# Optimization experiments

Measured on AMD Instinct MI355X. Metric: run time of the kernel, lower is better.

## Reference

```python
import jax, jax.numpy as jnp
import numpy as np
import math

B, L, D, P = 2, 2048, 256, 32

def _lin_init(key, fan_in, shape):
    return jax.random.normal(key, shape, dtype=jnp.float32) / np.float32(math.sqrt(fan_in))

def setup_inputs() -> dict:
    key = jax.random.key(0)
    ks = jax.random.split(key, 16)
    return {
        "x": jax.random.normal(ks[0], (B, L, D), dtype=jnp.float32),
        "pos_phases": jax.random.normal(ks[1], (L, P), dtype=jnp.float32) * np.float32(math.pi),
        "w_pos_value": _lin_init(ks[2], D, (D, D)), "b_pos_value": jnp.zeros((D,), jnp.float32),
        "w_key": _lin_init(ks[3], D, (D, P)), "b_key": jnp.zeros((P,), jnp.float32),
        "w_kv": _lin_init(ks[4], D, (D, D)), "b_kv": jnp.zeros((D,), jnp.float32),
        "w_vg1": _lin_init(ks[5], 2 * D, (2 * D, D)), "b_vg1": jnp.zeros((D,), jnp.float32),
        "w_vg2": _lin_init(ks[6], D, (D, 1)), "b_vg2": jnp.zeros((1,), jnp.float32),
        "w_bg1": _lin_init(ks[7], D, (D, D // 2)), "b_bg1": jnp.zeros((D // 2,), jnp.float32),
        "w_bg2": _lin_init(ks[8], D // 2, (D // 2, 2)), "b_bg2": jnp.zeros((2,), jnp.float32),
        "ln_r_g": jnp.ones((D,), jnp.float32), "ln_r_b": jnp.zeros((D,), jnp.float32),
        "w_r1": _lin_init(ks[9], D, (D, 2 * D)), "b_r1": jnp.zeros((2 * D,), jnp.float32),
        "w_r2": _lin_init(ks[10], 2 * D, (2 * D, D)), "b_r2": jnp.zeros((D,), jnp.float32),
        "ln_o_g": jnp.ones((D,), jnp.float32), "ln_o_b": jnp.zeros((D,), jnp.float32),
        "w_out": _lin_init(ks[11], D, (D, D)), "b_out": jnp.zeros((D,), jnp.float32),
    }

def _ln(z, g, b, eps=1e-5):
    mu = z.mean(-1, keepdims=True)
    var = ((z - mu) ** 2).mean(-1, keepdims=True)
    return (z - mu) * jax.lax.rsqrt(var + eps) * g + b

def _shift1(z):
    # torch.roll(shifts=1, dims=1) then zero first position == shift right with zero pad
    return jnp.concatenate([jnp.zeros_like(z[:, :1]), z[:, :-1]], axis=1)

def reference(x, pos_phases, w_pos_value, b_pos_value, w_key, b_key, w_kv, b_kv,
              w_vg1, b_vg1, w_vg2, b_vg2, w_bg1, b_bg1, w_bg2, b_bg2,
              ln_r_g, ln_r_b, w_r1, b_r1, w_r2, b_r2, ln_o_g, ln_o_b, w_out, b_out):
    Bv, Lv, Dv = x.shape
    Pv = pos_phases.shape[1]
    inv_sqrt_p = np.float32(1.0 / math.sqrt(Pv))

    # --- positional memory ---
    pos_phasors = jnp.exp(1j * pos_phases)                      # (L,P) complex64
    pos_values = (x @ w_pos_value + b_pos_value).astype(jnp.complex64)  # (B,L,D)
    pos_bound = pos_phasors[None, :, :, None] * pos_values[:, :, None, :]  # (B,L,P,D)
    pos_memory = jnp.cumsum(pos_bound, axis=1)
    pos_query = jnp.exp(-1j * pos_phases)                       # (L,P)
    pos_retrieved = (pos_memory * pos_query[None, :, :, None]).sum(axis=2).real * inv_sqrt_p

    # --- content-based KV memory ---
    key_phases = jnp.tanh(x @ w_key + b_key) * np.float32(math.pi)  # (B,L,P)
    key_phasors = jnp.exp(1j * key_phases)
    kv_values = (x @ w_kv + b_kv).astype(jnp.complex64)         # (B,L,D)

    x_shifted = _shift1(x)
    gate_input = jnp.concatenate([x, x_shifted], axis=-1)       # (B,L,2D)
    h = jax.nn.gelu(gate_input @ w_vg1 + b_vg1, approximate=False)
    value_gates = jax.nn.sigmoid(h @ w_vg2 + b_vg2)             # (B,L,1)

    key_phasors_shifted = _shift1(key_phasors)                  # (B,L,P)
    kv_bound = (key_phasors_shifted[..., None] * kv_values[:, :, None, :]) \
               * value_gates[:, :, :, None].astype(jnp.complex64)  # (B,L,P,D)
    kv_memory = jnp.cumsum(kv_bound, axis=1)
    gate_cumsum = jnp.maximum(jnp.cumsum(value_gates, axis=1), 1.0)  # (B,L,1)
    kv_query = jnp.exp(-1j * key_phases)                        # (B,L,P)
    kv_retrieved = (kv_memory * kv_query[..., None]).sum(axis=2).real
    kv_retrieved = kv_retrieved / (jnp.sqrt(gate_cumsum) * np.float32(math.sqrt(Pv)))

    # --- blend, refine, output ---
    bg_h = jax.nn.gelu(x @ w_bg1 + b_bg1, approximate=False)
    blend = jax.nn.softmax(bg_h @ w_bg2 + b_bg2, axis=-1)       # (B,L,2)
    blended = blend[..., 0:1] * pos_retrieved + blend[..., 1:2] * kv_retrieved

    refined = jax.nn.gelu(_ln(blended, ln_r_g, ln_r_b) @ w_r1 + b_r1, approximate=False) @ w_r2 + b_r2
    return x + (_ln(refined, ln_o_g, ln_o_b) @ w_out + b_out)
```

## Files before the change

kernel.cpp:

```cpp
#include <hip/hip_runtime.h>
#include <math.h>

#define B_ 2
#define L_ 2048
#define D_ 256
#define P_ 32
#define NC_ 32
#define CL_ 64

#define INV_SQRT_P 0.17677669529663687f
#define PI_F 3.14159265358979323846f

typedef __attribute__((ext_vector_type(8))) short bf16x8;
typedef __attribute__((ext_vector_type(4))) float f32x4;

__device__ __forceinline__ float gelu_exact(float x){
    return 0.5f * x * (1.0f + erff(x * 0.70710678118654752f));
}

__device__ __forceinline__ unsigned short f2bf(float f){
    unsigned int u = __float_as_uint(f);
    u += 0x7FFFu + ((u >> 16) & 1u);
    return (unsigned short)(u >> 16);
}

__device__ __forceinline__ float bf2f(unsigned short u){
    return __uint_as_float(((unsigned int)u) << 16);
}

__global__ __launch_bounds__(256) void k_prep(
    const float* __restrict__ pos_phases,
    const float* __restrict__ w_pv, const float* __restrict__ w_kv,
    const float* __restrict__ w_vg1, const float* __restrict__ w_bg1,
    const float* __restrict__ w_r1, const float* __restrict__ w_r2,
    const float* __restrict__ w_out, const float* __restrict__ w_key,
    unsigned short* __restrict__ wq,
    float* __restrict__ cpos, float* __restrict__ spos)
{
    int id = blockIdx.x * 256 + threadIdx.x;
    if (id < 630784){
        const float* src; int N; int local;
        if (id < 65536)       { src = w_pv;  N = 256; local = id; }
        else if (id < 131072) { src = w_kv;  N = 256; local = id - 65536; }
        else if (id < 262144) { src = w_vg1; N = 256; local = id - 131072; }
        else if (id < 294912) { src = w_bg1; N = 128; local = id - 262144; }
        else if (id < 425984) { src = w_r1;  N = 512; local = id - 294912; }
        else if (id < 557056) { src = w_r2;  N = 256; local = id - 425984; }
        else if (id < 622592) { src = w_out; N = 256; local = id - 557056; }
        else                  { src = w_key; N = 32;  local = id - 622592; }
        int j = local & 7, lane = (local >> 3) & 63, tile = local >> 9;
        int NT = N >> 4;
        int nt = tile % NT, kt = tile / NT;
        int row = kt * 32 + ((lane >> 4) << 3) + j;
        int col = nt * 16 + (lane & 15);
        wq[id] = f2bf(src[(size_t)row * N + col]);
    } else {
        int idx = id - 630784;
        float s, c;
        sincosf(pos_phases[idx], &s, &c);
        cpos[idx] = c;
        spos[idx] = s;
    }
}

__global__ __launch_bounds__(512) void k_proj(
    const float* __restrict__ x,
    const unsigned short* __restrict__ wq,
    const float* __restrict__ b_pv, const float* __restrict__ b_kv,
    const float* __restrict__ b_vg1,
    const float* __restrict__ w_vg2, const float* __restrict__ b_vg2,
    const float* __restrict__ b_bg1,
    const float* __restrict__ w_bg2, const float* __restrict__ b_bg2,
    const float* __restrict__ b_key,
    unsigned short* __restrict__ pvb, unsigned short* __restrict__ kvvb,
    float* __restrict__ ck, float* __restrict__ sk,
    float* __restrict__ vg, float* __restrict__ blend0, float* __restrict__ blend1)
{
    __shared__ float hbuf[16][257];
    __shared__ float kvbuf[16][257];
    __shared__ float bhbuf[16][129];
    __shared__ float kph[16][33];
    __shared__ float red[16][17], red2[16][17], red3[16][17];
    __shared__ float vgs[16];

    const int i = threadIdx.x;
    const int lane = i & 63, w = i >> 6;
    const int b = blockIdx.x >> 7, lt = blockIdx.x & 127, l0 = lt * 16;
    const int g = lane >> 4, c = lane & 15;

    bf16x8 xa[8], xs[8];
    {
        int row  = l0 + (lane & 15);
        int rowp = row - 1;
        const float* xr = x + (size_t)(b * L_ + row) * D_ + ((lane >> 4) << 3);
        #pragma unroll
        for (int kt = 0; kt < 8; ++kt){
            float4 a0 = *(const float4*)(xr + kt * 32);
            float4 a1 = *(const float4*)(xr + kt * 32 + 4);
            bf16x8 v;
            v[0] = (short)f2bf(a0.x); v[1] = (short)f2bf(a0.y);
            v[2] = (short)f2bf(a0.z); v[3] = (short)f2bf(a0.w);
            v[4] = (short)f2bf(a1.x); v[5] = (short)f2bf(a1.y);
            v[6] = (short)f2bf(a1.z); v[7] = (short)f2bf(a1.w);
            xa[kt] = v;
        }
        if (rowp >= 0){
            const float* xp = x + (size_t)(b * L_ + rowp) * D_ + ((lane >> 4) << 3);
            #pragma unroll
            for (int kt = 0; kt < 8; ++kt){
                float4 a0 = *(const float4*)(xp + kt * 32);
                float4 a1 = *(const float4*)(xp + kt * 32 + 4);
                bf16x8 v;
                v[0] = (short)f2bf(a0.x); v[1] = (short)f2bf(a0.y);
                v[2] = (short)f2bf(a0.z); v[3] = (short)f2bf(a0.w);
                v[4] = (short)f2bf(a1.x); v[5] = (short)f2bf(a1.y);
                v[6] = (short)f2bf(a1.z); v[7] = (short)f2bf(a1.w);
                xs[kt] = v;
            }
        } else {
            #pragma unroll
            for (int kt = 0; kt < 8; ++kt){
                bf16x8 v;
                #pragma unroll
                for (int j = 0; j < 8; ++j) v[j] = 0;
                xs[kt] = v;
            }
        }
    }

    const unsigned short* wpv  = wq;
    const unsigned short* wkv  = wq + 65536;
    const unsigned short* wvg1 = wq + 131072;
    const unsigned short* wbg1 = wq + 262144;
    const unsigned short* wkey = wq + 622592;

    for (int jb = w; jb < 58; jb += 8){
        f32x4 acc = {0.f, 0.f, 0.f, 0.f};
        if (jb < 2){
            int nt = jb;
            #pragma unroll
            for (int kt = 0; kt < 8; ++kt){
                bf16x8 bf = *(const bf16x8*)(wkey + (kt * 2 + nt) * 512 + lane * 8);
                acc = __builtin_amdgcn_mfma_f32_16x16x32_bf16(xa[kt], bf, acc, 0, 0, 0);
            }
            float bb = b_key[nt * 16 + c];
            #pragma unroll
            for (int r = 0; r < 4; ++r)
                kph[4 * g + r][nt * 16 + c] = acc[r] + bb;
        } else if (jb < 18){
            int nt = jb - 2;
            #pragma unroll
            for (int kt = 0; kt < 8; ++kt){
                bf16x8 bf = *(const bf16x8*)(wpv + (kt * 16 + nt) * 512 + lane * 8);
                acc = __builtin_amdgcn_mfma_f32_16x16x32_bf16(xa[kt], bf, acc, 0, 0, 0);
            }
            float bb = b_pv[nt * 16 + c];
            #pragma unroll
            for (int r = 0; r < 4; ++r)
                pvb[(size_t)(b * L_ + l0 + 4 * g + r) * D_ + nt * 16 + c] = f2bf(acc[r] + bb);
        } else if (jb < 34){
            int nt = jb - 18;
            #pragma unroll
            for (int kt = 0; kt < 8; ++kt){
                bf16x8 bf = *(const bf16x8*)(wkv + (kt * 16 + nt) * 512 + lane * 8);
                acc = __builtin_amdgcn_mfma_f32_16x16x32_bf16(xa[kt], bf, acc, 0, 0, 0);
            }
            float bb = b_kv[nt * 16 + c];
            #pragma unroll
            for (int r = 0; r < 4; ++r)
                kvbuf[4 * g + r][nt * 16 + c] = acc[r] + bb;
        } else if (jb < 50){
            int nt = jb - 34;
            #pragma unroll
            for (int kt = 0; kt < 8; ++kt){
                bf16x8 bf = *(const bf16x8*)(wvg1 + (kt * 16 + nt) * 512 + lane * 8);
                acc = __builtin_amdgcn_mfma_f32_16x16x32_bf16(xa[kt], bf, acc, 0, 0, 0);
            }
            #pragma unroll
            for (int kt = 8; kt < 16; ++kt){
                bf16x8 bf = *(const bf16x8*)(wvg1 + (kt * 16 + nt) * 512 + lane * 8);
                acc = __builtin_amdgcn_mfma_f32_16x16x32_bf16(xs[kt - 8], bf, acc, 0, 0, 0);
            }
            float bb = b_vg1[nt * 16 + c];
            #pragma unroll
            for (int r = 0; r < 4; ++r)
                hbuf[4 * g + r][nt * 16 + c] = gelu_exact(acc[r] + bb);
        } else {
            int nt = jb - 50;
            #pragma unroll
            for (int kt = 0; kt < 8; ++kt){
                bf16x8 bf = *(const bf16x8*)(wbg1 + (kt * 8 + nt) * 512 + lane * 8);
                acc = __builtin_amdgcn_mfma_f32_16x16x32_bf16(xa[kt], bf, acc, 0, 0, 0);
            }
            float bb = b_bg1[nt * 16 + c];
            #pragma unroll
            for (int r = 0; r < 4; ++r)
                bhbuf[4 * g + r][nt * 16 + c] = gelu_exact(acc[r] + bb);
        }
    }
    __syncthreads();

    {
        int t = i >> 5, p = i & 31;
        float a = tanhf(kph[t][p]) * PI_F;
        float s, cc;
        sincosf(a, &s, &cc);
        ck[(size_t)(b * L_ + l0 + t) * P_ + p] = cc;
        sk[(size_t)(b * L_ + l0 + t) * P_ + p] = s;
    }

    if (i < 256){
        int t = i >> 4, c2 = i & 15;
        float s = 0.f;
        #pragma unroll
        for (int m = 0; m < 16; ++m){ int dd = c2 + 16 * m; s += hbuf[t][dd] * w_vg2[dd]; }
        red[t][c2] = s;
    } else {
        int ii = i - 256;
        int t = ii >> 4, c2 = ii & 15;
        float s0 = 0.f, s1 = 0.f;
        #pragma unroll
        for (int m = 0; m < 8; ++m){
            int jj = c2 + 16 * m;
            float v = bhbuf[t][jj];
            s0 += v * w_bg2[jj * 2 + 0];
            s1 += v * w_bg2[jj * 2 + 1];
        }
        red2[t][c2] = s0; red3[t][c2] = s1;
    }
    __syncthreads();
    if (i < 16){
        float s = 0.f;
        #pragma unroll
        for (int c2 = 0; c2 < 16; ++c2) s += red[i][c2];
        s += b_vg2[0];
        float gv = 1.0f / (1.0f + expf(-s));
        vg[b * L_ + l0 + i] = gv;
        vgs[i] = gv;
    } else if (i < 32){
        int t = i - 16;
        float s0 = 0.f, s1 = 0.f;
        #pragma unroll
        for (int c2 = 0; c2 < 16; ++c2){ s0 += red2[t][c2]; s1 += red3[t][c2]; }
        s0 += b_bg2[0]; s1 += b_bg2[1];
        float mx = fmaxf(s0, s1);
        float e0 = expf(s0 - mx), e1 = expf(s1 - mx);
        float inv = 1.0f / (e0 + e1);
        blend0[b * L_ + l0 + t] = e0 * inv;
        blend1[b * L_ + l0 + t] = e1 * inv;
    }
    __syncthreads();

    {
        int d = i & 255, tg = i >> 8;
        #pragma unroll
        for (int m = 0; m < 8; ++m){
            int tok = tg * 8 + m;
            kvvb[(size_t)(b * L_ + l0 + tok) * D_ + d] = f2bf(kvbuf[tok][d] * vgs[tok]);
        }
    }
}

__global__ __launch_bounds__(256) void k_scan1(
    const float* __restrict__ cpos, const float* __restrict__ spos,
    const float* __restrict__ ck, const float* __restrict__ sk,
    const unsigned short* __restrict__ pvb, const unsigned short* __restrict__ kvvb,
    const float* __restrict__ vg,
    float* __restrict__ posSr, float* __restrict__ posSi,
    float* __restrict__ kvSr, float* __restrict__ kvSi,
    float* __restrict__ rnorm)
{
    const int z = blockIdx.z;
    const int c = blockIdx.x, b = blockIdx.y;
    const int i = threadIdx.x;
    if (z == 8){
        if (c != 0) return;
        float loc[8];
        float run = 0.f;
        #pragma unroll
        for (int m = 0; m < 8; ++m){ run += vg[b * L_ + i * 8 + m]; loc[m] = run; }
        __shared__ float part[256];
        part[i] = run;
        __syncthreads();
        for (int off = 1; off < 256; off <<= 1){
            float t = (i >= off) ? part[i - off] : 0.0f;
            __syncthreads();
            part[i] += t;
            __syncthreads();
        }
        float excl = part[i] - run;
        #pragma unroll
        for (int m = 0; m < 8; ++m){
            float gc = fmaxf(excl + loc[m], 1.0f);
            rnorm[b * L_ + i * 8 + m] = rsqrtf(gc) * INV_SQRT_P;
        }
        return;
    }
    const int type = z >> 2, pg = z & 3;
    const int d = i;
    const int p0 = pg * 8;
    float Sr[8], Si[8];
    #pragma unroll
    for (int j = 0; j < 8; ++j){ Sr[j] = 0.f; Si[j] = 0.f; }

    if (type == 0){
        for (int l = 0; l < CL_; ++l){
            int row = c * CL_ + l;
            float v = bf2f(pvb[(size_t)(b * L_ + row) * D_ + d]);
            float4 c0 = *(const float4*)(cpos + row * P_ + p0);
            float4 c1 = *(const float4*)(cpos + row * P_ + p0 + 4);
            float4 s0 = *(const float4*)(spos + row * P_ + p0);
            float4 s1 = *(const float4*)(spos + row * P_ + p0 + 4);
            Sr[0] = fmaf(c0.x, v, Sr[0]); Si[0] = fmaf(s0.x, v, Si[0]);
            Sr[1] = fmaf(c0.y, v, Sr[1]); Si[1] = fmaf(s0.y, v, Si[1]);
            Sr[2] = fmaf(c0.z, v, Sr[2]); Si[2] = fmaf(s0.z, v, Si[2]);
            Sr[3] = fmaf(c0.w, v, Sr[3]); Si[3] = fmaf(s0.w, v, Si[3]);
            Sr[4] = fmaf(c1.x, v, Sr[4]); Si[4] = fmaf(s1.x, v, Si[4]);
            Sr[5] = fmaf(c1.y, v, Sr[5]); Si[5] = fmaf(s1.y, v, Si[5]);
            Sr[6] = fmaf(c1.z, v, Sr[6]); Si[6] = fmaf(s1.z, v, Si[6]);
            Sr[7] = fmaf(c1.w, v, Sr[7]); Si[7] = fmaf(s1.w, v, Si[7]);
        }
        #pragma unroll
        for (int j = 0; j < 8; ++j){
            size_t o = (size_t)((b * NC_ + c) * P_ + p0 + j) * D_ + d;
            posSr[o] = Sr[j]; posSi[o] = Si[j];
        }
    } else {
        float pc[8], ps[8];
        int srow = c * CL_ - 1;
        if (srow >= 0){
            float4 c0 = *(const float4*)(ck + ((size_t)b * L_ + srow) * P_ + p0);
            float4 c1 = *(const float4*)(ck + ((size_t)b * L_ + srow) * P_ + p0 + 4);
            float4 s0 = *(const float4*)(sk + ((size_t)b * L_ + srow) * P_ + p0);
            float4 s1 = *(const float4*)(sk + ((size_t)b * L_ + srow) * P_ + p0 + 4);
            pc[0]=c0.x; pc[1]=c0.y; pc[2]=c0.z; pc[3]=c0.w;
            pc[4]=c1.x; pc[5]=c1.y; pc[6]=c1.z; pc[7]=c1.w;
            ps[0]=s0.x; ps[1]=s0.y; ps[2]=s0.z; ps[3]=s0.w;
            ps[4]=s1.x; ps[5]=s1.y; ps[6]=s1.z; ps[7]=s1.w;
        } else {
            #pragma unroll
            for (int j = 0; j < 8; ++j){ pc[j] = 0.f; ps[j] = 0.f; }
        }
        for (int l = 0; l < CL_; ++l){
            int row = c * CL_ + l;
            float vv = bf2f(kvvb[(size_t)(b * L_ + row) * D_ + d]);
            float4 c0 = *(const float4*)(ck + ((size_t)b * L_ + row) * P_ + p0);
            float4 c1 = *(const float4*)(ck + ((size_t)b * L_ + row) * P_ + p0 + 4);
            float4 s0 = *(const float4*)(sk + ((size_t)b * L_ + row) * P_ + p0);
            float4 s1 = *(const float4*)(sk + ((size_t)b * L_ + row) * P_ + p0 + 4);
            #pragma unroll
            for (int j = 0; j < 8; ++j){
                Sr[j] = fmaf(pc[j], vv, Sr[j]);
                Si[j] = fmaf(ps[j], vv, Si[j]);
            }
            pc[0]=c0.x; pc[1]=c0.y; pc[2]=c0.z; pc[3]=c0.w;
            pc[4]=c1.x; pc[5]=c1.y; pc[6]=c1.z; pc[7]=c1.w;
            ps[0]=s0.x; ps[1]=s0.y; ps[2]=s0.z; ps[3]=s0.w;
            ps[4]=s1.x; ps[5]=s1.y; ps[6]=s1.z; ps[7]=s1.w;
        }
        #pragma unroll
        for (int j = 0; j < 8; ++j){
            size_t o = (size_t)((b * NC_ + c) * P_ + p0 + j) * D_ + d;
            kvSr[o] = Sr[j]; kvSi[o] = Si[j];
        }
    }
}

__global__ __launch_bounds__(256) void k_prefix(
    float* __restrict__ posSr, float* __restrict__ posSi,
    float* __restrict__ kvSr, float* __restrict__ kvSi)
{
    __shared__ float4 tot_s[64][4];
    const int colLocal = threadIdx.x >> 2, seg = threadIdx.x & 3;
    const int col = blockIdx.x * 64 + colLocal;
    const int a = col >> 12;
    const int rem = col & 4095;
    const int b = rem >> 11;
    const int pd = (rem & 2047) * 4;
    float* A = (a == 0) ? posSr : (a == 1) ? posSi : (a == 2) ? kvSr : kvSi;
    float* base = A + (size_t)b * NC_ * (P_ * D_) + pd;

    float4 t[8];
    #pragma unroll
    for (int k = 0; k < 8; ++k)
        t[k] = *(const float4*)(base + (size_t)(seg * 8 + k) * (P_ * D_));
    float4 tot = {0.f, 0.f, 0.f, 0.f};
    #pragma unroll
    for (int k = 0; k < 8; ++k){
        tot.x += t[k].x; tot.y += t[k].y; tot.z += t[k].z; tot.w += t[k].w;
    }
    tot_s[colLocal][seg] = tot;
    __syncthreads();
    float4 run = {0.f, 0.f, 0.f, 0.f};
    #pragma unroll
    for (int s = 0; s < 3; ++s){
        if (s < seg){
            float4 v = tot_s[colLocal][s];
            run.x += v.x; run.y += v.y; run.z += v.z; run.w += v.w;
        }
    }
    #pragma unroll
    for (int k = 0; k < 8; ++k){
        float4 cur = t[k];
        *(float4*)(base + (size_t)(seg * 8 + k) * (P_ * D_)) = run;
        run.x += cur.x; run.y += cur.y; run.z += cur.z; run.w += cur.w;
    }
}

__global__ __launch_bounds__(256) void k_retrieve(
    const float* __restrict__ cpos, const float* __restrict__ spos,
    const float* __restrict__ ck, const float* __restrict__ sk,
    const unsigned short* __restrict__ pvb, const unsigned short* __restrict__ kvvb,
    const float* __restrict__ rnorm,
    const float* __restrict__ posSr, const float* __restrict__ posSi,
    const float* __restrict__ kvSr, const float* __restrict__ kvSi,
    unsigned short* __restrict__ posretb, unsigned short* __restrict__ kvretb)
{
    const int z = blockIdx.z;
    const int c = blockIdx.x, b = blockIdx.y;
    const int type = z >> 2, dquad = z & 3;
    const int lane = threadIdx.x & 63, wv = threadIdx.x >> 6;
    const int pg = lane >> 4, dl = lane & 15;
    const int d = dquad * 64 + wv * 16 + dl;
    const int p0 = pg * 8;

    float Sr[8], Si[8];

    if (type == 0){
        #pragma unroll
        for (int j = 0; j < 8; ++j){
            size_t o = (size_t)((b * NC_ + c) * P_ + p0 + j) * D_ + d;
            Sr[j] = posSr[o]; Si[j] = posSi[o];
        }
        for (int l = 0; l < CL_; ++l){
            int row = c * CL_ + l;
            float v = bf2f(pvb[(size_t)(b * L_ + row) * D_ + d]);
            float4 c0 = *(const float4*)(cpos + row * P_ + p0);
            float4 c1 = *(const float4*)(cpos + row * P_ + p0 + 4);
            float4 s0 = *(const float4*)(spos + row * P_ + p0);
            float4 s1 = *(const float4*)(spos + row * P_ + p0 + 4);
            float r0 = 0.f, r1 = 0.f, r2 = 0.f, r3 = 0.f;
            Sr[0] = fmaf(c0.x, v, Sr[0]); r0 = fmaf(c0.x, Sr[0], r0);
            Si[0] = fmaf(s0.x, v, Si[0]); r1 = fmaf(s0.x, Si[0], r1);
            Sr[1] = fmaf(c0.y, v, Sr[1]); r2 = fmaf(c0.y, Sr[1], r2);
            Si[1] = fmaf(s0.y, v, Si[1]); r3 = fmaf(s0.y, Si[1], r3);
            Sr[2] = fmaf(c0.z, v, Sr[2]); r0 = fmaf(c0.z, Sr[2], r0);
            Si[2] = fmaf(s0.z, v, Si[2]); r1 = fmaf(s0.z, Si[2], r1);
            Sr[3] = fmaf(c0.w, v, Sr[3]); r2 = fmaf(c0.w, Sr[3], r2);
            Si[3] = fmaf(s0.w, v, Si[3]); r3 = fmaf(s0.w, Si[3], r3);
            Sr[4] = fmaf(c1.x, v, Sr[4]); r0 = fmaf(c1.x, Sr[4], r0);
            Si[4] = fmaf(s1.x, v, Si[4]); r1 = fmaf(s1.x, Si[4], r1);
            Sr[5] = fmaf(c1.y, v, Sr[5]); r2 = fmaf(c1.y, Sr[5], r2);
            Si[5] = fmaf(s1.y, v, Si[5]); r3 = fmaf(s1.y, Si[5], r3);
            Sr[6] = fmaf(c1.z, v, Sr[6]); r0 = fmaf(c1.z, Sr[6], r0);
            Si[6] = fmaf(s1.z, v, Si[6]); r1 = fmaf(s1.z, Si[6], r1);
            Sr[7] = fmaf(c1.w, v, Sr[7]); r2 = fmaf(c1.w, Sr[7], r2);
            Si[7] = fmaf(s1.w, v, Si[7]); r3 = fmaf(s1.w, Si[7], r3);
            float r = (r0 + r1) + (r2 + r3);
            r += __shfl_xor(r, 16, 64);
            r += __shfl_xor(r, 32, 64);
            if (pg == 0)
                posretb[(size_t)(b * L_ + row) * D_ + d] = f2bf(r * INV_SQRT_P);
        }
    } else {
        #pragma unroll
        for (int j = 0; j < 8; ++j){
            size_t o = (size_t)((b * NC_ + c) * P_ + p0 + j) * D_ + d;
            Sr[j] = kvSr[o]; Si[j] = kvSi[o];
        }
        float pc[8], ps[8];
        int srow = c * CL_ - 1;
        if (srow >= 0){
            float4 c0 = *(const float4*)(ck + ((size_t)b * L_ + srow) * P_ + p0);
            float4 c1 = *(const float4*)(ck + ((size_t)b * L_ + srow) * P_ + p0 + 4);
            float4 s0 = *(const float4*)(sk + ((size_t)b * L_ + srow) * P_ + p0);
            float4 s1 = *(const float4*)(sk + ((size_t)b * L_ + srow) * P_ + p0 + 4);
            pc[0]=c0.x; pc[1]=c0.y; pc[2]=c0.z; pc[3]=c0.w;
            pc[4]=c1.x; pc[5]=c1.y; pc[6]=c1.z; pc[7]=c1.w;
            ps[0]=s0.x; ps[1]=s0.y; ps[2]=s0.z; ps[3]=s0.w;
            ps[4]=s1.x; ps[5]=s1.y; ps[6]=s1.z; ps[7]=s1.w;
        } else {
            #pragma unroll
            for (int j = 0; j < 8; ++j){ pc[j] = 0.f; ps[j] = 0.f; }
        }
        for (int l = 0; l < CL_; ++l){
            int row = c * CL_ + l;
            float vv = bf2f(kvvb[(size_t)(b * L_ + row) * D_ + d]);
            float rn = rnorm[b * L_ + row];
            float4 c0 = *(const float4*)(ck + ((size_t)b * L_ + row) * P_ + p0);
            float4 c1 = *(const float4*)(ck + ((size_t)b * L_ + row) * P_ + p0 + 4);
            float4 s0 = *(const float4*)(sk + ((size_t)b * L_ + row) * P_ + p0);
            float4 s1 = *(const float4*)(sk + ((size_t)b * L_ + row) * P_ + p0 + 4);
            float qc[8], qs[8];
            qc[0]=c0.x; qc[1]=c0.y; qc[2]=c0.z; qc[3]=c0.w;
            qc[4]=c1.x; qc[5]=c1.y; qc[6]=c1.z; qc[7]=c1.w;
            qs[0]=s0.x; qs[1]=s0.y; qs[2]=s0.z; qs[3]=s0.w;
            qs[4]=s1.x; qs[5]=s1.y; qs[6]=s1.z; qs[7]=s1.w;
            float r0 = 0.f, r1 = 0.f, r2 = 0.f, r3 = 0.f;
            #pragma unroll
            for (int j = 0; j < 8; ++j){
                Sr[j] = fmaf(pc[j], vv, Sr[j]);
                Si[j] = fmaf(ps[j], vv, Si[j]);
                if (j & 1){ r2 = fmaf(qc[j], Sr[j], r2); r3 = fmaf(qs[j], Si[j], r3); }
                else      { r0 = fmaf(qc[j], Sr[j], r0); r1 = fmaf(qs[j], Si[j], r1); }
                pc[j] = qc[j]; ps[j] = qs[j];
            }
            float r = (r0 + r1) + (r2 + r3);
            r += __shfl_xor(r, 16, 64);
            r += __shfl_xor(r, 32, 64);
            if (pg == 0)
                kvretb[(size_t)(b * L_ + row) * D_ + d] = f2bf(r * rn);
        }
    }
}

__global__ __launch_bounds__(512) void k_final(
    const float* __restrict__ x,
    const unsigned short* __restrict__ posretb, const unsigned short* __restrict__ kvretb,
    const float* __restrict__ blend0, const float* __restrict__ blend1,
    const unsigned short* __restrict__ wq,
    const float* __restrict__ ln_r_g, const float* __restrict__ ln_r_b,
    const float* __restrict__ b_r1, const float* __restrict__ b_r2,
    const float* __restrict__ ln_o_g, const float* __restrict__ ln_o_b,
    const float* __restrict__ b_out,
    float* __restrict__ out)
{
    __shared__ float zbuf[16][257];
    __shared__ __align__(16) unsigned short aA[8][512];
    __shared__ __align__(16) unsigned short aH[16][512];
    __shared__ float red[16][17], red2[16][17];
    __shared__ float mu[16], rs[16];

    const int i = threadIdx.x, lane = i & 63, w = i >> 6;
    const int b = blockIdx.x >> 7, l0 = (blockIdx.x & 127) * 16;
    const int g = lane >> 4, c = lane & 15;
    const unsigned short* wr1  = wq + 294912;
    const unsigned short* wr2  = wq + 425984;
    const unsigned short* wout = wq + 557056;

    {
        int t = i >> 5, c0 = (i & 31) * 8;
        size_t base = (size_t)(b * L_ + l0 + t) * D_ + c0;
        float w0 = blend0[b * L_ + l0 + t], w1 = blend1[b * L_ + l0 + t];
        bf16x8 pp = *(const bf16x8*)(posretb + base);
        bf16x8 kk = *(const bf16x8*)(kvretb + base);
        #pragma unroll
        for (int m = 0; m < 8; ++m)
            zbuf[t][c0 + m] = w0 * bf2f((unsigned short)pp[m])
                            + w1 * bf2f((unsigned short)kk[m]);
    }
    __syncthreads();

    if (i < 256){
        int t = i >> 4, c2 = i & 15;
        float s = 0.f, s2 = 0.f;
        #pragma unroll
        for (int m = 0; m < 16; ++m){ float v = zbuf[t][c2 + 16 * m]; s += v; s2 += v * v; }
        red[t][c2] = s; red2[t][c2] = s2;
    }
    __syncthreads();
    if (i < 16){
        float s = 0.f, s2 = 0.f;
        #pragma unroll
        for (int c2 = 0; c2 < 16; ++c2){ s += red[i][c2]; s2 += red2[i][c2]; }
        float mean = s * (1.0f / 256.0f);
        float var  = s2 * (1.0f / 256.0f) - mean * mean;
        mu[i] = mean; rs[i] = rsqrtf(var + 1e-5f);
    }
    __syncthreads();

    {
        int kt = i >> 6;
        int t2 = lane & 15, kb = kt * 32 + ((lane >> 4) << 3);
        float m_ = mu[t2], r_ = rs[t2];
        bf16x8 v8;
        #pragma unroll
        for (int j = 0; j < 8; ++j){
            int k = kb + j;
            float v = (zbuf[t2][k] - m_) * r_ * ln_r_g[k] + ln_r_b[k];
            v8[j] = (short)f2bf(v);
        }
        *(bf16x8*)&aA[kt][lane * 8] = v8;
    }
    __syncthreads();

    {
        bf16x8 afr[8];
        #pragma unroll
        for (int kt = 0; kt < 8; ++kt) afr[kt] = *(const bf16x8*)&aA[kt][lane * 8];
        for (int q = 0; q < 4; ++q){
            int nt = w + 8 * q;
            f32x4 acc = {0.f, 0.f, 0.f, 0.f};
            #pragma unroll
            for (int kt = 0; kt < 8; ++kt){
                bf16x8 bf = *(const bf16x8*)(wr1 + (kt * 32 + nt) * 512 + lane * 8);
                acc = __builtin_amdgcn_mfma_f32_16x16x32_bf16(afr[kt], bf, acc, 0, 0, 0);
            }
            float bb = b_r1[nt * 16 + c];
            #pragma unroll
            for (int r = 0; r < 4; ++r){
                float hv = gelu_exact(acc[r] + bb);
                int t = 4 * g + r, hcol = nt * 16 + c;
                int kt2 = hcol >> 5, kk = hcol & 31;
                int lane2 = ((kk >> 3) << 4) + t, j2 = kk & 7;
                aH[kt2][lane2 * 8 + j2] = f2bf(hv);
            }
        }
    }
    __syncthreads();

    {
        bf16x8 hfr[16];
        #pragma unroll
        for (int kt = 0; kt < 16; ++kt) hfr[kt] = *(const bf16x8*)&aH[kt][lane * 8];
        for (int q = 0; q < 2; ++q){
            int nt = w + 8 * q;
            f32x4 acc = {0.f, 0.f, 0.f, 0.f};
            #pragma unroll
            for (int kt = 0; kt < 16; ++kt){
                bf16x8 bf = *(const bf16x8*)(wr2 + (kt * 16 + nt) * 512 + lane * 8);
                acc = __builtin_amdgcn_mfma_f32_16x16x32_bf16(hfr[kt], bf, acc, 0, 0, 0);
            }
            float bb = b_r2[nt * 16 + c];
            #pragma unroll
            for (int r = 0; r < 4; ++r)
                zbuf[4 * g + r][nt * 16 + c] = acc[r] + bb;
        }
    }
    __syncthreads();

    if (i < 256){
        int t = i >> 4, c2 = i & 15;
        float s = 0.f, s2 = 0.f;
        #pragma unroll
        for (int m = 0; m < 16; ++m){ float v = zbuf[t][c2 + 16 * m]; s += v; s2 += v * v; }
        red[t][c2] = s; red2[t][c2] = s2;
    }
    __syncthreads();
    if (i < 16){
        float s = 0.f, s2 = 0.f;
        #pragma unroll
        for (int c2 = 0; c2 < 16; ++c2){ s += red[i][c2]; s2 += red2[i][c2]; }
        float mean = s * (1.0f / 256.0f);
        float var  = s2 * (1.0f / 256.0f) - mean * mean;
        mu[i] = mean; rs[i] = rsqrtf(var + 1e-5f);
    }
    __syncthreads();

    {
        int kt = i >> 6;
        int t2 = lane & 15, kb = kt * 32 + ((lane >> 4) << 3);
        float m_ = mu[t2], r_ = rs[t2];
        bf16x8 v8;
        #pragma unroll
        for (int j = 0; j < 8; ++j){
            int k = kb + j;
            float v = (zbuf[t2][k] - m_) * r_ * ln_o_g[k] + ln_o_b[k];
            v8[j] = (short)f2bf(v);
        }
        *(bf16x8*)&aA[kt][lane * 8] = v8;
    }
    __syncthreads();

    {
        bf16x8 azr[8];
        #pragma unroll
        for (int kt = 0; kt < 8; ++kt) azr[kt] = *(const bf16x8*)&aA[kt][lane * 8];
        for (int q = 0; q < 2; ++q){
            int nt = w + 8 * q;
            f32x4 acc = {0.f, 0.f, 0.f, 0.f};
            #pragma unroll
            for (int kt = 0; kt < 8; ++kt){
                bf16x8 bf = *(const bf16x8*)(wout + (kt * 16 + nt) * 512 + lane * 8);
                acc = __builtin_amdgcn_mfma_f32_16x16x32_bf16(azr[kt], bf, acc, 0, 0, 0);
            }
            float bb = b_out[nt * 16 + c];
            #pragma unroll
            for (int r = 0; r < 4; ++r){
                size_t o = (size_t)(b * L_ + l0 + 4 * g + r) * D_ + nt * 16 + c;
                out[o] = x[o] + acc[r] + bb;
            }
        }
    }
}

extern "C" void kernel_launch(void* const* d_in, const int* in_sizes, int n_in,
                              void* d_out, int out_size, void* d_ws, size_t ws_size,
                              hipStream_t stream) {
    const float* x          = (const float*)d_in[0];
    const float* pos_phases = (const float*)d_in[1];
    const float* w_pv       = (const float*)d_in[2];
    const float* b_pv       = (const float*)d_in[3];
    const float* w_key      = (const float*)d_in[4];
    const float* b_key      = (const float*)d_in[5];
    const float* w_kv       = (const float*)d_in[6];
    const float* b_kv       = (const float*)d_in[7];
    const float* w_vg1      = (const float*)d_in[8];
    const float* b_vg1      = (const float*)d_in[9];
    const float* w_vg2      = (const float*)d_in[10];
    const float* b_vg2      = (const float*)d_in[11];
    const float* w_bg1      = (const float*)d_in[12];
    const float* b_bg1      = (const float*)d_in[13];
    const float* w_bg2      = (const float*)d_in[14];
    const float* b_bg2      = (const float*)d_in[15];
    const float* ln_r_g     = (const float*)d_in[16];
    const float* ln_r_b     = (const float*)d_in[17];
    const float* w_r1       = (const float*)d_in[18];
    const float* b_r1       = (const float*)d_in[19];
    const float* w_r2       = (const float*)d_in[20];
    const float* b_r2       = (const float*)d_in[21];
    const float* ln_o_g     = (const float*)d_in[22];
    const float* ln_o_b     = (const float*)d_in[23];
    const float* w_out      = (const float*)d_in[24];
    const float* b_out      = (const float*)d_in[25];
    float* out = (float*)d_out;

    float* ws = (float*)d_ws;
    size_t off = 0;
    float* cpos   = ws + off; off += (size_t)L_ * P_;
    float* spos   = ws + off; off += (size_t)L_ * P_;
    float* ck     = ws + off; off += (size_t)B_ * L_ * P_;
    float* sk     = ws + off; off += (size_t)B_ * L_ * P_;
    float* vg     = ws + off; off += (size_t)B_ * L_;
    float* rnorm  = ws + off; off += (size_t)B_ * L_;
    float* blend0 = ws + off; off += (size_t)B_ * L_;
    float* blend1 = ws + off; off += (size_t)B_ * L_;
    float* posSr  = ws + off; off += (size_t)B_ * NC_ * P_ * D_;
    float* posSi  = ws + off; off += (size_t)B_ * NC_ * P_ * D_;
    float* kvSr   = ws + off; off += (size_t)B_ * NC_ * P_ * D_;
    float* kvSi   = ws + off; off += (size_t)B_ * NC_ * P_ * D_;
    unsigned short* wq      = (unsigned short*)(ws + off); off += 630784 / 2;
    unsigned short* pvb     = (unsigned short*)(ws + off); off += (size_t)B_ * L_ * D_ / 2;
    unsigned short* kvvb    = (unsigned short*)(ws + off); off += (size_t)B_ * L_ * D_ / 2;
    unsigned short* posretb = (unsigned short*)(ws + off); off += (size_t)B_ * L_ * D_ / 2;
    unsigned short* kvretb  = (unsigned short*)(ws + off); off += (size_t)B_ * L_ * D_ / 2;

    k_prep<<<2720, 256, 0, stream>>>(pos_phases,
        w_pv, w_kv, w_vg1, w_bg1, w_r1, w_r2, w_out, w_key,
        wq, cpos, spos);

    k_proj<<<B_ * 128, 512, 0, stream>>>(x, wq,
        b_pv, b_kv, b_vg1, w_vg2, b_vg2, b_bg1, w_bg2, b_bg2, b_key,
        pvb, kvvb, ck, sk, vg, blend0, blend1);

    k_scan1<<<dim3(NC_, B_, 9), 256, 0, stream>>>(cpos, spos, ck, sk, pvb, kvvb, vg,
                                                  posSr, posSi, kvSr, kvSi, rnorm);

    k_prefix<<<256, 256, 0, stream>>>(posSr, posSi, kvSr, kvSi);

    k_retrieve<<<dim3(NC_, B_, 8), 256, 0, stream>>>(cpos, spos, ck, sk, pvb, kvvb,
                                                     rnorm,
                                                     posSr, posSi, kvSr, kvSi,
                                                     posretb, kvretb);

    k_final<<<B_ * 128, 512, 0, stream>>>(x, posretb, kvretb, blend0, blend1, wq,
        ln_r_g, ln_r_b, b_r1, b_r2, ln_o_g, ln_o_b, b_out, out);
}
```

Baseline: 103.5 us.

## Split projection kernel into four block groups and double scan chunk count

```diff
diff --git a/kernel.cpp b/kernel.cpp
--- a/kernel.cpp
+++ b/kernel.cpp
@@ -5,8 +5,8 @@
 #define L_ 2048
 #define D_ 256
 #define P_ 32
-#define NC_ 32
-#define CL_ 64
+#define NC_ 64
+#define CL_ 32
 
 #define INV_SQRT_P 0.17677669529663687f
 #define PI_F 3.14159265358979323846f
@@ -77,21 +77,20 @@
     float* __restrict__ vg, float* __restrict__ blend0, float* __restrict__ blend1)
 {
     __shared__ float hbuf[16][257];
-    __shared__ float kvbuf[16][257];
-    __shared__ float bhbuf[16][129];
-    __shared__ float kph[16][33];
-    __shared__ float red[16][17], red2[16][17], red3[16][17];
-    __shared__ float vgs[16];
+    __shared__ float red[16][17], red2[16][17];
+
+    float (*bhbuf)[129] = (float (*)[129])&hbuf[0][0];
+    float (*kph)[33]    = (float (*)[33])&hbuf[8][128];
 
     const int i = threadIdx.x;
     const int lane = i & 63, w = i >> 6;
     const int b = blockIdx.x >> 7, lt = blockIdx.x & 127, l0 = lt * 16;
+    const int grp = blockIdx.y;
     const int g = lane >> 4, c = lane & 15;
 
     bf16x8 xa[8], xs[8];
     {
         int row  = l0 + (lane & 15);
-        int rowp = row - 1;
         const float* xr = x + (size_t)(b * L_ + row) * D_ + ((lane >> 4) << 3);
         #pragma unroll
         for (int kt = 0; kt < 8; ++kt){
@@ -104,26 +103,29 @@
             v[6] = (short)f2bf(a1.z); v[7] = (short)f2bf(a1.w);
             xa[kt] = v;
         }
-        if (rowp >= 0){
-            const float* xp = x + (size_t)(b * L_ + rowp) * D_ + ((lane >> 4) << 3);
-            #pragma unroll
-            for (int kt = 0; kt < 8; ++kt){
-                float4 a0 = *(const float4*)(xp + kt * 32);
-                float4 a1 = *(const float4*)(xp + kt * 32 + 4);
-                bf16x8 v;
-                v[0] = (short)f2bf(a0.x); v[1] = (short)f2bf(a0.y);
-                v[2] = (short)f2bf(a0.z); v[3] = (short)f2bf(a0.w);
-                v[4] = (short)f2bf(a1.x); v[5] = (short)f2bf(a1.y);
-                v[6] = (short)f2bf(a1.z); v[7] = (short)f2bf(a1.w);
-                xs[kt] = v;
-            }
-        } else {
-            #pragma unroll
-            for (int kt = 0; kt < 8; ++kt){
-                bf16x8 v;
+        if (grp == 2){
+            int rowp = row - 1;
+            if (rowp >= 0){
+                const float* xp = x + (size_t)(b * L_ + rowp) * D_ + ((lane >> 4) << 3);
                 #pragma unroll
-                for (int j = 0; j < 8; ++j) v[j] = 0;
-                xs[kt] = v;
+                for (int kt = 0; kt < 8; ++kt){
+                    float4 a0 = *(const float4*)(xp + kt * 32);
+                    float4 a1 = *(const float4*)(xp + kt * 32 + 4);
+                    bf16x8 v;
+                    v[0] = (short)f2bf(a0.x); v[1] = (short)f2bf(a0.y);
+                    v[2] = (short)f2bf(a0.z); v[3] = (short)f2bf(a0.w);
+                    v[4] = (short)f2bf(a1.x); v[5] = (short)f2bf(a1.y);
+                    v[6] = (short)f2bf(a1.z); v[7] = (short)f2bf(a1.w);
+                    xs[kt] = v;
+                }
+            } else {
+                #pragma unroll
+                for (int kt = 0; kt < 8; ++kt){
+                    bf16x8 v;
+                    #pragma unroll
+                    for (int j = 0; j < 8; ++j) v[j] = 0;
+                    xs[kt] = v;
+                }
             }
         }
     }
@@ -134,21 +136,11 @@
     const unsigned short* wbg1 = wq + 262144;
     const unsigned short* wkey = wq + 622592;
 
-    for (int jb = w; jb < 58; jb += 8){
-        f32x4 acc = {0.f, 0.f, 0.f, 0.f};
-        if (jb < 2){
-            int nt = jb;
-            #pragma unroll
-            for (int kt = 0; kt < 8; ++kt){
-                bf16x8 bf = *(const bf16x8*)(wkey + (kt * 2 + nt) * 512 + lane * 8);
-                acc = __builtin_amdgcn_mfma_f32_16x16x32_bf16(xa[kt], bf, acc, 0, 0, 0);
-            }
-            float bb = b_key[nt * 16 + c];
-            #pragma unroll
-            for (int r = 0; r < 4; ++r)
-                kph[4 * g + r][nt * 16 + c] = acc[r] + bb;
-        } else if (jb < 18){
-            int nt = jb - 2;
+    if (grp == 0){
+        #pragma unroll
+        for (int q = 0; q < 2; ++q){
+            int nt = w + 8 * q;
+            f32x4 acc = {0.f, 0.f, 0.f, 0.f};
             #pragma unroll
             for (int kt = 0; kt < 8; ++kt){
                 bf16x8 bf = *(const bf16x8*)(wpv + (kt * 16 + nt) * 512 + lane * 8);
@@ -158,8 +150,12 @@
             #pragma unroll
             for (int r = 0; r < 4; ++r)
                 pvb[(size_t)(b * L_ + l0 + 4 * g + r) * D_ + nt * 16 + c] = f2bf(acc[r] + bb);
-        } else if (jb < 34){
-            int nt = jb - 18;
+        }
+    } else if (grp == 1){
+        #pragma unroll
+        for (int q = 0; q < 2; ++q){
+            int nt = w + 8 * q;
+            f32x4 acc = {0.f, 0.f, 0.f, 0.f};
             #pragma unroll
             for (int kt = 0; kt < 8; ++kt){
                 bf16x8 bf = *(const bf16x8*)(wkv + (kt * 16 + nt) * 512 + lane * 8);
@@ -168,9 +164,13 @@
             float bb = b_kv[nt * 16 + c];
             #pragma unroll
             for (int r = 0; r < 4; ++r)
-                kvbuf[4 * g + r][nt * 16 + c] = acc[r] + bb;
-        } else if (jb < 50){
-            int nt = jb - 34;
+                kvvb[(size_t)(b * L_ + l0 + 4 * g + r) * D_ + nt * 16 + c] = f2bf(acc[r] + bb);
+        }
+    } else if (grp == 2){
+        #pragma unroll
+        for (int q = 0; q < 2; ++q){
+            int nt = w + 8 * q;
+            f32x4 acc = {0.f, 0.f, 0.f, 0.f};
             #pragma unroll
             for (int kt = 0; kt < 8; ++kt){
                 bf16x8 bf = *(const bf16x8*)(wvg1 + (kt * 16 + nt) * 512 + lane * 8);
@@ -185,78 +185,82 @@
             #pragma unroll
             for (int r = 0; r < 4; ++r)
                 hbuf[4 * g + r][nt * 16 + c] = gelu_exact(acc[r] + bb);
-        } else {
-            int nt = jb - 50;
-            #pragma unroll
-            for (int kt = 0; kt < 8; ++kt){
-                bf16x8 bf = *(const bf16x8*)(wbg1 + (kt * 8 + nt) * 512 + lane * 8);
-                acc = __builtin_amdgcn_mfma_f32_16x16x32_bf16(xa[kt], bf, acc, 0, 0, 0);
-            }
-            float bb = b_bg1[nt * 16 + c];
-            #pragma unroll
-            for (int r = 0; r < 4; ++r)
-                bhbuf[4 * g + r][nt * 16 + c] = gelu_exact(acc[r] + bb);
-        }
-    }
-    __syncthreads();
-
-    {
-        int t = i >> 5, p = i & 31;
-        float a = tanhf(kph[t][p]) * PI_F;
-        float s, cc;
-        sincosf(a, &s, &cc);
-        ck[(size_t)(b * L_ + l0 + t) * P_ + p] = cc;
-        sk[(size_t)(b * L_ + l0 + t) * P_ + p] = s;
-    }
-
-    if (i < 256){
-        int t = i >> 4, c2 = i & 15;
-        float s = 0.f;
-        #pragma unroll
-        for (int m = 0; m < 16; ++m){ int dd = c2 + 16 * m; s += hbuf[t][dd] * w_vg2[dd]; }
-        red[t][c2] = s;
+        }
+        __syncthreads();
+        if (i < 256){
+            int t = i >> 4, c2 = i & 15;
+            float s = 0.f;
+            #pragma unroll
+            for (int m = 0; m < 16; ++m){ int dd = c2 + 16 * m; s += hbuf[t][dd] * w_vg2[dd]; }
+            red[t][c2] = s;
+        }
+        __syncthreads();
+        if (i < 16){
+            float s = 0.f;
+            #pragma unroll
+            for (int c2 = 0; c2 < 16; ++c2) s += red[i][c2];
+            s += b_vg2[0];
+            vg[b * L_ + l0 + i] = 1.0f / (1.0f + expf(-s));
+        }
     } else {
-        int ii = i - 256;
-        int t = ii >> 4, c2 = ii & 15;
-        float s0 = 0.f, s1 = 0.f;
-        #pragma unroll
-        for (int m = 0; m < 8; ++m){
-            int jj = c2 + 16 * m;
-            float v = bhbuf[t][jj];
-            s0 += v * w_bg2[jj * 2 + 0];
-            s1 += v * w_bg2[jj * 2 + 1];
-        }
-        red2[t][c2] = s0; red3[t][c2] = s1;
-    }
-    __syncthreads();
-    if (i < 16){
-        float s = 0.f;
-        #pragma unroll
-        for (int c2 = 0; c2 < 16; ++c2) s += red[i][c2];
-        s += b_vg2[0];
-        float gv = 1.0f / (1.0f + expf(-s));
-        vg[b * L_ + l0 + i] = gv;
-        vgs[i] = gv;
-    } else if (i < 32){
-        int t = i - 16;
-        float s0 = 0.f, s1 = 0.f;
-        #pragma unroll
-        for (int c2 = 0; c2 < 16; ++c2){ s0 += red2[t][c2]; s1 += red3[t][c2]; }
-        s0 += b_bg2[0]; s1 += b_bg2[1];
-        float mx = fmaxf(s0, s1);
-        float e0 = expf(s0 - mx), e1 = expf(s1 - mx);
-        float inv = 1.0f / (e0 + e1);
-        blend0[b * L_ + l0 + t] = e0 * inv;
-        blend1[b * L_ + l0 + t] = e1 * inv;
-    }
-    __syncthreads();
-
-    {
-        int d = i & 255, tg = i >> 8;
-        #pragma unroll
-        for (int m = 0; m < 8; ++m){
-            int tok = tg * 8 + m;
-            kvvb[(size_t)(b * L_ + l0 + tok) * D_ + d] = f2bf(kvbuf[tok][d] * vgs[tok]);
+        for (int jb = w; jb < 10; jb += 8){
+            f32x4 acc = {0.f, 0.f, 0.f, 0.f};
+            if (jb < 2){
+                int nt = jb;
+                #pragma unroll
+                for (int kt = 0; kt < 8; ++kt){
+                    bf16x8 bf = *(const bf16x8*)(wkey + (kt * 2 + nt) * 512 + lane * 8);
+                    acc = __builtin_amdgcn_mfma_f32_16x16x32_bf16(xa[kt], bf, acc, 0, 0, 0);
+                }
+                float bb = b_key[nt * 16 + c];
+                #pragma unroll
+                for (int r = 0; r < 4; ++r)
+                    kph[4 * g + r][nt * 16 + c] = acc[r] + bb;
+            } else {
+                int nt = jb - 2;
+                #pragma unroll
+                for (int kt = 0; kt < 8; ++kt){
+                    bf16x8 bf = *(const bf16x8*)(wbg1 + (kt * 8 + nt) * 512 + lane * 8);
+                    acc = __builtin_amdgcn_mfma_f32_16x16x32_bf16(xa[kt], bf, acc, 0, 0, 0);
+                }
+                float bb = b_bg1[nt * 16 + c];
+                #pragma unroll
+                for (int r = 0; r < 4; ++r)
+                    bhbuf[4 * g + r][nt * 16 + c] = gelu_exact(acc[r] + bb);
+            }
+        }
+        __syncthreads();
+        {
+            int t = i >> 5, p = i & 31;
+            float a = tanhf(kph[t][p]) * PI_F;
+            float s, cc;
+            sincosf(a, &s, &cc);
+            ck[(size_t)(b * L_ + l0 + t) * P_ + p] = cc;
+            sk[(size_t)(b * L_ + l0 + t) * P_ + p] = s;
+        }
+        if (i < 128){
+            int t = i >> 3, c2 = i & 7;
+            float s0 = 0.f, s1 = 0.f;
+            #pragma unroll
+            for (int m = 0; m < 16; ++m){
+                int jj = c2 + 8 * m;
+                float v = bhbuf[t][jj];
+                s0 += v * w_bg2[jj * 2 + 0];
+                s1 += v * w_bg2[jj * 2 + 1];
+            }
+            red[t][c2] = s0; red2[t][c2] = s1;
+        }
+        __syncthreads();
+        if (i < 16){
+            float s0 = 0.f, s1 = 0.f;
+            #pragma unroll
+            for (int c2 = 0; c2 < 8; ++c2){ s0 += red[i][c2]; s1 += red2[i][c2]; }
+            s0 += b_bg2[0]; s1 += b_bg2[1];
+            float mx = fmaxf(s0, s1);
+            float e0 = expf(s0 - mx), e1 = expf(s1 - mx);
+            float inv = 1.0f / (e0 + e1);
+            blend0[b * L_ + l0 + i] = e0 * inv;
+            blend1[b * L_ + l0 + i] = e1 * inv;
         }
     }
 }
@@ -343,7 +347,7 @@
         }
         for (int l = 0; l < CL_; ++l){
             int row = c * CL_ + l;
-            float vv = bf2f(kvvb[(size_t)(b * L_ + row) * D_ + d]);
+            float vv = bf2f(kvvb[(size_t)(b * L_ + row) * D_ + d]) * vg[b * L_ + row];
             float4 c0 = *(const float4*)(ck + ((size_t)b * L_ + row) * P_ + p0);
             float4 c1 = *(const float4*)(ck + ((size_t)b * L_ + row) * P_ + p0 + 4);
             float4 s0 = *(const float4*)(sk + ((size_t)b * L_ + row) * P_ + p0);
@@ -370,9 +374,9 @@
     float* __restrict__ posSr, float* __restrict__ posSi,
     float* __restrict__ kvSr, float* __restrict__ kvSi)
 {
-    __shared__ float4 tot_s[64][4];
-    const int colLocal = threadIdx.x >> 2, seg = threadIdx.x & 3;
-    const int col = blockIdx.x * 64 + colLocal;
+    __shared__ float4 tot_s[32][8];
+    const int colLocal = threadIdx.x >> 3, seg = threadIdx.x & 7;
+    const int col = blockIdx.x * 32 + colLocal;
     const int a = col >> 12;
     const int rem = col & 4095;
     const int b = rem >> 11;
@@ -393,7 +397,7 @@
     __syncthreads();
     float4 run = {0.f, 0.f, 0.f, 0.f};
     #pragma unroll
-    for (int s = 0; s < 3; ++s){
+    for (int s = 0; s < 7; ++s){
         if (s < seg){
             float4 v = tot_s[colLocal][s];
             run.x += v.x; run.y += v.y; run.z += v.z; run.w += v.w;
@@ -411,7 +415,7 @@
     const float* __restrict__ cpos, const float* __restrict__ spos,
     const float* __restrict__ ck, const float* __restrict__ sk,
     const unsigned short* __restrict__ pvb, const unsigned short* __restrict__ kvvb,
-    const float* __restrict__ rnorm,
+    const float* __restrict__ vg, const float* __restrict__ rnorm,
     const float* __restrict__ posSr, const float* __restrict__ posSi,
     const float* __restrict__ kvSr, const float* __restrict__ kvSi,
     unsigned short* __restrict__ posretb, unsigned short* __restrict__ kvretb)
@@ -485,7 +489,7 @@
         }
         for (int l = 0; l < CL_; ++l){
             int row = c * CL_ + l;
-            float vv = bf2f(kvvb[(size_t)(b * L_ + row) * D_ + d]);
+            float vv = bf2f(kvvb[(size_t)(b * L_ + row) * D_ + d]) * vg[b * L_ + row];
             float rn = rnorm[b * L_ + row];
             float4 c0 = *(const float4*)(ck + ((size_t)b * L_ + row) * P_ + p0);
             float4 c1 = *(const float4*)(ck + ((size_t)b * L_ + row) * P_ + p0 + 4);
@@ -739,17 +743,17 @@
         w_pv, w_kv, w_vg1, w_bg1, w_r1, w_r2, w_out, w_key,
         wq, cpos, spos);
 
-    k_proj<<<B_ * 128, 512, 0, stream>>>(x, wq,
+    k_proj<<<dim3(B_ * 128, 4), 512, 0, stream>>>(x, wq,
         b_pv, b_kv, b_vg1, w_vg2, b_vg2, b_bg1, w_bg2, b_bg2, b_key,
         pvb, kvvb, ck, sk, vg, blend0, blend1);
 
     k_scan1<<<dim3(NC_, B_, 9), 256, 0, stream>>>(cpos, spos, ck, sk, pvb, kvvb, vg,
                                                   posSr, posSi, kvSr, kvSi, rnorm);
 
-    k_prefix<<<256, 256, 0, stream>>>(posSr, posSi, kvSr, kvSi);
+    k_prefix<<<512, 256, 0, stream>>>(posSr, posSi, kvSr, kvSi);
 
     k_retrieve<<<dim3(NC_, B_, 8), 256, 0, stream>>>(cpos, spos, ck, sk, pvb, kvvb,
-                                                     rnorm,
+                                                     vg, rnorm,
                                                      posSr, posSi, kvSr, kvSi,
                                                      posretb, kvretb);
 
```

Result: faster. 101.2 us (-2.2%).
